# Kernel optimization log

Measured on AMD Instinct MI355X. Metric: run time of the kernel, lower is better.

## Reference

```python
import jax, jax.numpy as jnp
import numpy as np

IN_DIMS = 512
TOKEN_DIM = 512
NUM_HEADS = 1
D = TOKEN_DIM * NUM_HEADS
SCALE = TOKEN_DIM ** (-0.5)
EPS = 1e-12  # torch F.normalize default


def _l2norm(v, axis):
    n = jnp.sqrt(jnp.sum(v * v, axis=axis, keepdims=True))
    return v / jnp.maximum(n, EPS)


def setup_inputs() -> dict:
    key = jax.random.key(0)
    ks = jax.random.split(key, 10)
    B, C, H, W = 64, IN_DIMS, 28, 28
    s_in = IN_DIMS ** -0.5
    s_d = D ** -0.5
    return {
        "x": jax.random.normal(ks[0], (B, C, H, W), jnp.float32),
        "Wq": jax.random.normal(ks[1], (IN_DIMS, D), jnp.float32) * s_in,
        "bq": jax.random.normal(ks[2], (D,), jnp.float32) * 0.01,
        "Wk": jax.random.normal(ks[3], (IN_DIMS, D), jnp.float32) * s_in,
        "bk": jax.random.normal(ks[4], (D,), jnp.float32) * 0.01,
        "w_g": jax.random.normal(ks[5], (D, 1), jnp.float32),
        "Wp": jax.random.normal(ks[6], (D, D), jnp.float32) * s_d,
        "bp": jax.random.normal(ks[7], (D,), jnp.float32) * 0.01,
        "Wf": jax.random.normal(ks[8], (D, TOKEN_DIM), jnp.float32) * s_d,
        "bf": jax.random.normal(ks[9], (TOKEN_DIM,), jnp.float32) * 0.01,
    }


def reference(x, Wq, bq, Wk, bk, w_g, Wp, bp, Wf, bf):
    B, C, H, W = x.shape
    t = x.reshape(B, C, H * W).transpose(0, 2, 1)          # [B, N, C]
    query = _l2norm(t @ Wq + bq, axis=-1)                  # [B, N, D]
    k = _l2norm(t @ Wk + bk, axis=-1)                      # [B, N, D]
    attn = _l2norm((query @ w_g) * SCALE, axis=1)          # [B, N, 1], normalized over tokens
    ctx = jnp.sum(attn * query, axis=1, keepdims=True)     # [B, 1, D] global context
    out = (ctx * k) @ Wp + bp + query                      # [B, N, D]
    out = out @ Wf + bf                                    # [B, N, TOKEN_DIM]
    return out.transpose(0, 2, 1).reshape(B, -1, H, W)
```

## Files before the change

### kernel.cpp

```cpp
#include <hip/hip_runtime.h>

#define EPSN 1e-12f
#define SCALE_F 0.044194173824159216f

typedef __bf16 bf16x8 __attribute__((ext_vector_type(8)));
typedef __bf16 bf16x4 __attribute__((ext_vector_type(4)));
typedef float  f32x4  __attribute__((ext_vector_type(4)));

__device__ __forceinline__ void gld16(const void* src, void* dst) {
  __builtin_amdgcn_global_load_lds(
      (const __attribute__((address_space(1))) unsigned int*)src,
      (__attribute__((address_space(3))) unsigned int*)dst, 16, 0, 0);
}

__global__ __launch_bounds__(256) void k_prep_t(const float* __restrict__ Wq,
                                                const float* __restrict__ Wk,
                                                __bf16* __restrict__ WqT,
                                                __bf16* __restrict__ WkT) {
  __shared__ float Tq[32][33], Tk[32][33];
  const int c0 = blockIdx.x * 32, d0 = blockIdx.y * 32;
  const int dx = threadIdx.x, cy = threadIdx.y;
  #pragma unroll
  for (int p = 0; p < 4; ++p) {
    int c = cy + p * 8;
    Tq[c][dx] = Wq[(size_t)(c0 + c) * 512 + d0 + dx];
    Tk[c][dx] = Wk[(size_t)(c0 + c) * 512 + d0 + dx];
  }
  __syncthreads();
  #pragma unroll
  for (int p = 0; p < 4; ++p) {
    int d = cy + p * 8;
    WqT[(size_t)(d0 + d) * 512 + c0 + dx] = (__bf16)Tq[dx][d];
    WkT[(size_t)(d0 + d) * 512 + c0 + dx] = (__bf16)Tk[dx][d];
  }
}

__global__ __launch_bounds__(512) void k_prep_w(const float* __restrict__ Wp,
                                                const float* __restrict__ Wf,
                                                const float* __restrict__ bp,
                                                const float* __restrict__ bfv,
                                                __bf16* __restrict__ WcT,
                                                float* __restrict__ bpf) {
  int kk = blockIdx.x;
  int d  = threadIdx.x;
  float a0 = 0.f, a1 = 0.f, a2 = 0.f, a3 = 0.f;
  for (int c = 0; c < 512; c += 4) {
    a0 = fmaf(Wp[kk * 512 + c],     Wf[(size_t)c * 512 + d],         a0);
    a1 = fmaf(Wp[kk * 512 + c + 1], Wf[(size_t)(c + 1) * 512 + d],   a1);
    a2 = fmaf(Wp[kk * 512 + c + 2], Wf[(size_t)(c + 2) * 512 + d],   a2);
    a3 = fmaf(Wp[kk * 512 + c + 3], Wf[(size_t)(c + 3) * 512 + d],   a3);
  }
  WcT[(size_t)d * 1024 + kk]       = (__bf16)((a0 + a1) + (a2 + a3));
  WcT[(size_t)d * 1024 + 512 + kk] = (__bf16)Wf[(size_t)kk * 512 + d];
  if (kk == 0) {
    float b0 = 0.f, b1 = 0.f;
    for (int c = 0; c < 512; c += 2) {
      b0 = fmaf(bp[c],     Wf[(size_t)c * 512 + d],       b0);
      b1 = fmaf(bp[c + 1], Wf[(size_t)(c + 1) * 512 + d], b1);
    }
    bpf[d] = b0 + b1 + bfv[d];
  }
}

__global__ __launch_bounds__(512, 4) void k_qk(const float* __restrict__ x,
                                               const __bf16* __restrict__ WqT,
                                               const __bf16* __restrict__ WkT,
                                               const float* __restrict__ bq,
                                               const float* __restrict__ bk,
                                               const float* __restrict__ wg,
                                               __bf16* __restrict__ Qn,
                                               __bf16* __restrict__ Kn,
                                               float* __restrict__ pctx,
                                               float* __restrict__ pgsq) {
  __shared__ __align__(1024) unsigned char stg[36864];
  __shared__ float red[8][64], redG[8][64], invv[64], gs[64];
  const int t = threadIdx.x, lane = t & 63, w = t >> 6;
  const int li = lane & 15, lq = lane >> 4;
  const int n0 = blockIdx.x * 64, b = blockIdx.y, isK = blockIdx.z;
  const __bf16* Wt  = isK ? WkT : WqT;
  const float* bias = isK ? bk : bq;
  __bf16* dst       = isK ? Kn : Qn;

  const int stok = t & 63, scp = (t >> 6) * 4;
  const bool nv = (n0 + stok < 784);
  const float* xp = x + ((size_t)b * 512 + scp) * 784 + n0 + stok;
  const __bf16* wsrc = Wt + (size_t)((w * 4) * 16 + (lane >> 2)) * 512 + (lane & 3) * 8;

  f32x4 acc[4][4] = {};

  for (int ks = 0; ks < 16; ++ks) {
    const int k0 = ks * 32;
    #pragma unroll
    for (int i = 0; i < 4; ++i) {
      int r = w * 4 + i;
      gld16(wsrc + (size_t)i * 16 * 512 + k0, (void*)(stg + 4096 + r * 1024));
    }
    {
      float v0 = nv ? xp[(size_t)(k0 + 0) * 784] : 0.f;
      float v1 = nv ? xp[(size_t)(k0 + 1) * 784] : 0.f;
      float v2 = nv ? xp[(size_t)(k0 + 2) * 784] : 0.f;
      float v3 = nv ? xp[(size_t)(k0 + 3) * 784] : 0.f;
      bf16x4 v; v[0] = (__bf16)v0; v[1] = (__bf16)v1; v[2] = (__bf16)v2; v[3] = (__bf16)v3;
      *(bf16x4*)(stg + stok * 64 + scp * 2) = v;
    }
    __syncthreads();
    bf16x8 af[4];
    #pragma unroll
    for (int rb = 0; rb < 4; ++rb)
      af[rb] = *(const bf16x8*)(stg + (rb * 16 + li) * 64 + lq * 16);
    #pragma unroll
    for (int cb = 0; cb < 4; ++cb) {
      bf16x8 bf = *(const bf16x8*)(stg + 4096 + (w * 64 + cb * 16 + li) * 64 + lq * 16);
      #pragma unroll
      for (int rb = 0; rb < 4; ++rb)
        acc[rb][cb] = __builtin_amdgcn_mfma_f32_16x16x32_bf16(af[rb], bf, acc[rb][cb], 0, 0, 0);
    }
    __syncthreads();
  }

  float bv[4], wv[4];
  #pragma unroll
  for (int cb = 0; cb < 4; ++cb) {
    int col = w * 64 + cb * 16 + li;
    bv[cb] = bias[col];
    wv[cb] = isK ? 0.f : wg[col];
  }
  #pragma unroll
  for (int rb = 0; rb < 4; ++rb)
    #pragma unroll
    for (int cb = 0; cb < 4; ++cb)
      #pragma unroll
      for (int j = 0; j < 4; ++j)
        acc[rb][cb][j] += bv[cb];
  #pragma unroll
  for (int rb = 0; rb < 4; ++rb)
    #pragma unroll
    for (int j = 0; j < 4; ++j) {
      float ss = 0.f, sg = 0.f;
      #pragma unroll
      for (int cb = 0; cb < 4; ++cb) {
        float v = acc[rb][cb][j];
        ss = fmaf(v, v, ss); sg = fmaf(v, wv[cb], sg);
      }
      ss += __shfl_xor(ss, 1); ss += __shfl_xor(ss, 2); ss += __shfl_xor(ss, 4); ss += __shfl_xor(ss, 8);
      sg += __shfl_xor(sg, 1); sg += __shfl_xor(sg, 2); sg += __shfl_xor(sg, 4); sg += __shfl_xor(sg, 8);
      if (li == 0) {
        int row = rb * 16 + lq * 4 + j;
        red[w][row] = ss; redG[w][row] = sg;
      }
    }
  __syncthreads();
  if (t < 64) {
    float ss = 0.f, sg = 0.f;
    #pragma unroll
    for (int wv2 = 0; wv2 < 8; ++wv2) { ss += red[wv2][t]; sg += redG[wv2][t]; }
    float iv = 1.f / fmaxf(sqrtf(ss), EPSN);
    invv[t] = iv;
    if (!isK) {
      float gv = (n0 + t < 784) ? sg * iv : 0.f;
      gs[t] = gv;
      float pg = gv * gv;
      pg += __shfl_xor(pg, 1);  pg += __shfl_xor(pg, 2);  pg += __shfl_xor(pg, 4);
      pg += __shfl_xor(pg, 8);  pg += __shfl_xor(pg, 16); pg += __shfl_xor(pg, 32);
      if (t == 0) pgsq[b * 13 + blockIdx.x] = pg;
    }
  }
  __syncthreads();
  float pc[4] = {0.f, 0.f, 0.f, 0.f};
  #pragma unroll
  for (int rb = 0; rb < 4; ++rb)
    #pragma unroll
    for (int j = 0; j < 4; ++j) {
      int row = rb * 16 + lq * 4 + j;
      if (n0 + row < 784) {
        float iv = invv[row];
        float gr = isK ? 0.f : gs[row];
        size_t base = ((size_t)b * 784 + n0 + row) * 512 + w * 64 + li;
        #pragma unroll
        for (int cb = 0; cb < 4; ++cb) {
          float qv = acc[rb][cb][j] * iv;
          dst[base + cb * 16] = (__bf16)qv;
          pc[cb] = fmaf(gr, qv, pc[cb]);
        }
      }
    }
  if (!isK) {
    #pragma unroll
    for (int cb = 0; cb < 4; ++cb) {
      pc[cb] += __shfl_xor(pc[cb], 16);
      pc[cb] += __shfl_xor(pc[cb], 32);
    }
    if (lq == 0) {
      #pragma unroll
      for (int cb = 0; cb < 4; ++cb)
        pctx[((size_t)b * 13 + blockIdx.x) * 512 + w * 64 + cb * 16 + li] = pc[cb];
    }
  }
}

__global__ __launch_bounds__(512) void k_ctx2(const float* __restrict__ pctx,
                                              const float* __restrict__ pgsq,
                                              float* __restrict__ ctx) {
  const int b = blockIdx.x, t = threadIdx.x;
  float tot = 0.f;
  #pragma unroll
  for (int i = 0; i < 13; ++i) tot += pgsq[b * 13 + i];
  float alpha = SCALE_F / fmaxf(sqrtf(tot) * SCALE_F, EPSN);
  float s = 0.f;
  #pragma unroll
  for (int i = 0; i < 13; ++i) s += pctx[((size_t)b * 13 + i) * 512 + t];
  ctx[(size_t)b * 512 + t] = alpha * s;
}

__global__ __launch_bounds__(512) void k_kc(__bf16* __restrict__ Kn,
                                            const float* __restrict__ ctx) {
  const int b = blockIdx.y;
  const int chunk = blockIdx.x * 512 + threadIdx.x;
  const int row = chunk >> 6;
  const int c8 = (chunk & 63) * 8;
  __bf16* p = Kn + ((size_t)b * 784 + row) * 512 + c8;
  const float* cp = ctx + b * 512 + c8;
  bf16x8 v = *(const bf16x8*)p;
  #pragma unroll
  for (int j = 0; j < 8; ++j) v[j] = (__bf16)((float)v[j] * cp[j]);
  *(bf16x8*)p = v;
}

__global__ __launch_bounds__(512, 4) void k_out(const __bf16* __restrict__ Qn,
                                                const __bf16* __restrict__ Kc,
                                                const __bf16* __restrict__ WcT,
                                                const float* __restrict__ bpf,
                                                float* __restrict__ out) {
  __shared__ __align__(1024) unsigned char stg[36864];
  const int t = threadIdx.x, lane = t & 63, w = t >> 6;
  const int li = lane & 15, lq = lane >> 4;
  const int n0 = blockIdx.x * 64, b = blockIdx.y;
  size_t grow = (size_t)b * 784 + n0 + (lane >> 2);
  f32x4 acc[4][4] = {};

  for (int ks = 0; ks < 32; ++ks) {
    const int k0 = ks * 32;
    const __bf16* Arow = (ks < 16) ? Kc : Qn;
    const int kA = (ks < 16) ? k0 : k0 - 512;
    #pragma unroll
    for (int i = 0; i < 5; ++i) {
      int r = w + i * 8;
      if (r < 36) {
        void* dstl = (void*)(stg + r * 1024);
        if (r < 4) {
          size_t gr = grow + r * 16;
          if (gr > 50175) gr = 50175;
          gld16(Arow + gr * 512 + kA + (lane & 3) * 8, dstl);
        } else {
          int dr = (r - 4) * 16 + (lane >> 2);
          gld16(WcT + (size_t)dr * 1024 + k0 + (lane & 3) * 8, dstl);
        }
      }
    }
    __syncthreads();
    bf16x8 af[4];
    #pragma unroll
    for (int rb = 0; rb < 4; ++rb)
      af[rb] = *(const bf16x8*)(stg + (rb * 16 + li) * 64 + lq * 16);
    #pragma unroll
    for (int cb = 0; cb < 4; ++cb) {
      bf16x8 bf = *(const bf16x8*)(stg + 4096 + (w * 64 + cb * 16 + li) * 64 + lq * 16);
      #pragma unroll
      for (int rb = 0; rb < 4; ++rb)
        acc[rb][cb] = __builtin_amdgcn_mfma_f32_16x16x32_bf16(af[rb], bf, acc[rb][cb], 0, 0, 0);
    }
    __syncthreads();
  }

  float bv[4];
  #pragma unroll
  for (int cb = 0; cb < 4; ++cb) bv[cb] = bpf[w * 64 + cb * 16 + li];
  #pragma unroll
  for (int rb = 0; rb < 4; ++rb) {
    int nrow = n0 + rb * 16 + lq * 4;
    if (nrow < 784) {
      #pragma unroll
      for (int cb = 0; cb < 4; ++cb) {
        f32x4 v;
        #pragma unroll
        for (int j = 0; j < 4; ++j) v[j] = acc[rb][cb][j] + bv[cb];
        *(f32x4*)&out[((size_t)b * 512 + w * 64 + cb * 16 + li) * 784 + nrow] = v;
      }
    }
  }
}

extern "C" void kernel_launch(void* const* d_in, const int* in_sizes, int n_in,
                              void* d_out, int out_size, void* d_ws, size_t ws_size,
                              hipStream_t stream) {
  const float* x   = (const float*)d_in[0];
  const float* Wq  = (const float*)d_in[1];
  const float* bq  = (const float*)d_in[2];
  const float* Wk  = (const float*)d_in[3];
  const float* bk  = (const float*)d_in[4];
  const float* wg  = (const float*)d_in[5];
  const float* Wp  = (const float*)d_in[6];
  const float* bp  = (const float*)d_in[7];
  const float* Wf  = (const float*)d_in[8];
  const float* bfv = (const float*)d_in[9];
  float* out = (float*)d_out;
  char* ws = (char*)d_ws;

  const size_t SZQN = (size_t)64 * 784 * 512 * 2;
  __bf16* Qn   = (__bf16*)(ws);
  __bf16* Kn   = (__bf16*)(ws + SZQN);
  __bf16* WqT  = (__bf16*)(ws + 2 * SZQN);
  __bf16* WkT  = (__bf16*)(ws + 2 * SZQN + 524288);
  __bf16* WcT  = (__bf16*)(ws + 2 * SZQN + 2 * 524288);
  float*  bpf  = (float*) (ws + 2 * SZQN + 2 * 524288 + 1048576);
  float*  pctx = (float*) (ws + 2 * SZQN + 2 * 524288 + 1048576 + 2048);
  float*  pgsq = (float*) (ws + 2 * SZQN + 2 * 524288 + 1048576 + 2048 + 1703936);
  float*  ctx  = (float*) (ws + 2 * SZQN + 2 * 524288 + 1048576 + 2048 + 1703936 + 4096);

  k_prep_t<<<dim3(16, 16),    dim3(32, 8), 0, stream>>>(Wq, Wk, WqT, WkT);
  k_prep_w<<<dim3(512),       dim3(512),   0, stream>>>(Wp, Wf, bp, bfv, WcT, bpf);
  k_qk    <<<dim3(13, 64, 2), dim3(512),   0, stream>>>(x, WqT, WkT, bq, bk, wg, Qn, Kn, pctx, pgsq);
  k_ctx2  <<<dim3(64),        dim3(512),   0, stream>>>(pctx, pgsq, ctx);
  k_kc    <<<dim3(98, 64),    dim3(512),   0, stream>>>(Kn, ctx);
  k_out   <<<dim3(13, 64),    dim3(512),   0, stream>>>(Qn, Kn, WcT, bpf, out);
}
```

Baseline: 347.2 us.

## Retile QK and output GEMMs to 128x128 tiles with deferred normalization

```diff
diff --git a/kernel.cpp b/kernel.cpp
--- a/kernel.cpp
+++ b/kernel.cpp
@@ -2,6 +2,7 @@
 
 #define EPSN 1e-12f
 #define SCALE_F 0.044194173824159216f
+#define MTOT 50176
 
 typedef __bf16 bf16x8 __attribute__((ext_vector_type(8)));
 typedef __bf16 bf16x4 __attribute__((ext_vector_type(4)));
@@ -41,76 +42,82 @@
                                                 const float* __restrict__ bfv,
                                                 __bf16* __restrict__ WcT,
                                                 float* __restrict__ bpf) {
-  int kk = blockIdx.x;
-  int d  = threadIdx.x;
-  float a0 = 0.f, a1 = 0.f, a2 = 0.f, a3 = 0.f;
-  for (int c = 0; c < 512; c += 4) {
-    a0 = fmaf(Wp[kk * 512 + c],     Wf[(size_t)c * 512 + d],         a0);
-    a1 = fmaf(Wp[kk * 512 + c + 1], Wf[(size_t)(c + 1) * 512 + d],   a1);
-    a2 = fmaf(Wp[kk * 512 + c + 2], Wf[(size_t)(c + 2) * 512 + d],   a2);
-    a3 = fmaf(Wp[kk * 512 + c + 3], Wf[(size_t)(c + 3) * 512 + d],   a3);
-  }
-  WcT[(size_t)d * 1024 + kk]       = (__bf16)((a0 + a1) + (a2 + a3));
-  WcT[(size_t)d * 1024 + 512 + kk] = (__bf16)Wf[(size_t)kk * 512 + d];
-  if (kk == 0) {
-    float b0 = 0.f, b1 = 0.f;
-    for (int c = 0; c < 512; c += 2) {
-      b0 = fmaf(bp[c],     Wf[(size_t)c * 512 + d],       b0);
-      b1 = fmaf(bp[c + 1], Wf[(size_t)(c + 1) * 512 + d], b1);
-    }
-    bpf[d] = b0 + b1 + bfv[d];
-  }
-}
-
-__global__ __launch_bounds__(512, 4) void k_qk(const float* __restrict__ x,
-                                               const __bf16* __restrict__ WqT,
-                                               const __bf16* __restrict__ WkT,
-                                               const float* __restrict__ bq,
-                                               const float* __restrict__ bk,
-                                               const float* __restrict__ wg,
-                                               __bf16* __restrict__ Qn,
-                                               __bf16* __restrict__ Kn,
-                                               float* __restrict__ pctx,
-                                               float* __restrict__ pgsq) {
-  __shared__ __align__(1024) unsigned char stg[36864];
-  __shared__ float red[8][64], redG[8][64], invv[64], gs[64];
-  const int t = threadIdx.x, lane = t & 63, w = t >> 6;
-  const int li = lane & 15, lq = lane >> 4;
-  const int n0 = blockIdx.x * 64, b = blockIdx.y, isK = blockIdx.z;
-  const __bf16* Wt  = isK ? WkT : WqT;
-  const float* bias = isK ? bk : bq;
-  __bf16* dst       = isK ? Kn : Qn;
-
-  const int stok = t & 63, scp = (t >> 6) * 4;
-  const bool nv = (n0 + stok < 784);
-  const float* xp = x + ((size_t)b * 512 + scp) * 784 + n0 + stok;
-  const __bf16* wsrc = Wt + (size_t)((w * 4) * 16 + (lane >> 2)) * 512 + (lane & 3) * 8;
+  const int kk0 = blockIdx.x * 8;
+  const int d = threadIdx.x;
+  float acc[8] = {};
+  float bacc = 0.f;
+  const bool dobp = (blockIdx.x == 0);
+  for (int c = 0; c < 512; ++c) {
+    float wf = Wf[(size_t)c * 512 + d];
+    #pragma unroll
+    for (int i = 0; i < 8; ++i) acc[i] = fmaf(Wp[(size_t)(kk0 + i) * 512 + c], wf, acc[i]);
+    if (dobp) bacc = fmaf(bp[c], wf, bacc);
+  }
+  #pragma unroll
+  for (int i = 0; i < 8; ++i) {
+    WcT[(size_t)d * 1024 + kk0 + i]       = (__bf16)acc[i];
+    WcT[(size_t)d * 1024 + 512 + kk0 + i] = (__bf16)Wf[(size_t)(kk0 + i) * 512 + d];
+  }
+  if (dobp) bpf[d] = bacc + bfv[d];
+}
+
+__global__ __launch_bounds__(256, 3) void k_gemm(const float* __restrict__ x,
+                                                 const __bf16* __restrict__ WqT,
+                                                 const __bf16* __restrict__ WkT,
+                                                 const float* __restrict__ bq,
+                                                 const float* __restrict__ bk,
+                                                 const float* __restrict__ wg,
+                                                 __bf16* __restrict__ qraw,
+                                                 __bf16* __restrict__ kraw,
+                                                 float* __restrict__ psqQ,
+                                                 float* __restrict__ psqK,
+                                                 float* __restrict__ gdo) {
+  __shared__ __align__(1024) unsigned char As[8192], Bs[8192];
+  const int t = threadIdx.x, l = t & 63, w = t >> 6;
+  const int li = l & 15, lq = l >> 4;
+  const int p = blockIdx.x;
+  const int xq = p & 7, q2 = p >> 3;
+  const int m8 = q2 & 7;
+  const int g = (q2 >> 3) * 8 + xq;
+  const int b = g / 7, mt = g % 7;
+  const int qk = m8 >> 2, nt = m8 & 3;
+  const int m0 = mt * 128;
+  const __bf16* Wt = qk ? WkT : WqT;
+
+  const int r0 = 2 * w, r1 = r0 + 1;
+  int row0 = m0 + r0 * 16 + li; if (row0 > 783) row0 = 783;
+  int row1 = m0 + r1 * 16 + li; if (row1 > 783) row1 = 783;
+  const float* xp0 = x + ((size_t)b * 512 + lq * 8) * 784 + row0;
+  const float* xp1 = x + ((size_t)b * 512 + lq * 8) * 784 + row1;
+  const __bf16* wp0 = Wt + (size_t)(nt * 128 + r0 * 16 + li) * 512 + lq * 8;
+  const __bf16* wp1 = Wt + (size_t)(nt * 128 + r1 * 16 + li) * 512 + lq * 8;
 
   f32x4 acc[4][4] = {};
 
   for (int ks = 0; ks < 16; ++ks) {
     const int k0 = ks * 32;
-    #pragma unroll
-    for (int i = 0; i < 4; ++i) {
-      int r = w * 4 + i;
-      gld16(wsrc + (size_t)i * 16 * 512 + k0, (void*)(stg + 4096 + r * 1024));
-    }
+    gld16(wp0 + k0, Bs + r0 * 1024);
+    gld16(wp1 + k0, Bs + r1 * 1024);
     {
-      float v0 = nv ? xp[(size_t)(k0 + 0) * 784] : 0.f;
-      float v1 = nv ? xp[(size_t)(k0 + 1) * 784] : 0.f;
-      float v2 = nv ? xp[(size_t)(k0 + 2) * 784] : 0.f;
-      float v3 = nv ? xp[(size_t)(k0 + 3) * 784] : 0.f;
-      bf16x4 v; v[0] = (__bf16)v0; v[1] = (__bf16)v1; v[2] = (__bf16)v2; v[3] = (__bf16)v3;
-      *(bf16x4*)(stg + stok * 64 + scp * 2) = v;
+      float v0[8], v1[8];
+      #pragma unroll
+      for (int j = 0; j < 8; ++j) v0[j] = xp0[(size_t)(k0 + j) * 784];
+      #pragma unroll
+      for (int j = 0; j < 8; ++j) v1[j] = xp1[(size_t)(k0 + j) * 784];
+      bf16x8 a0, a1;
+      #pragma unroll
+      for (int j = 0; j < 8; ++j) { a0[j] = (__bf16)v0[j]; a1[j] = (__bf16)v1[j]; }
+      *(bf16x8*)(As + r0 * 1024 + l * 16) = a0;
+      *(bf16x8*)(As + r1 * 1024 + l * 16) = a1;
     }
     __syncthreads();
     bf16x8 af[4];
     #pragma unroll
     for (int rb = 0; rb < 4; ++rb)
-      af[rb] = *(const bf16x8*)(stg + (rb * 16 + li) * 64 + lq * 16);
+      af[rb] = *(const bf16x8*)(As + ((w & 1) * 4 + rb) * 1024 + l * 16);
     #pragma unroll
     for (int cb = 0; cb < 4; ++cb) {
-      bf16x8 bf = *(const bf16x8*)(stg + 4096 + (w * 64 + cb * 16 + li) * 64 + lq * 16);
+      bf16x8 bf = *(const bf16x8*)(Bs + ((w >> 1) * 4 + cb) * 1024 + l * 16);
       #pragma unroll
       for (int rb = 0; rb < 4; ++rb)
         acc[rb][cb] = __builtin_amdgcn_mfma_f32_16x16x32_bf16(af[rb], bf, acc[rb][cb], 0, 0, 0);
@@ -118,153 +125,169 @@
     __syncthreads();
   }
 
+  const float* bias = qk ? bk : bq;
+  __bf16* dst = qk ? kraw : qraw;
+  float* psq = qk ? psqK : psqQ;
+  const int colb = nt * 128 + (w >> 1) * 64;
+  const int cg = nt * 2 + (w >> 1);
   float bv[4], wv[4];
   #pragma unroll
   for (int cb = 0; cb < 4; ++cb) {
-    int col = w * 64 + cb * 16 + li;
+    int col = colb + cb * 16 + li;
     bv[cb] = bias[col];
-    wv[cb] = isK ? 0.f : wg[col];
+    wv[cb] = qk ? 0.f : wg[col];
   }
   #pragma unroll
   for (int rb = 0; rb < 4; ++rb)
     #pragma unroll
-    for (int cb = 0; cb < 4; ++cb)
-      #pragma unroll
-      for (int j = 0; j < 4; ++j)
-        acc[rb][cb][j] += bv[cb];
-  #pragma unroll
-  for (int rb = 0; rb < 4; ++rb)
-    #pragma unroll
     for (int j = 0; j < 4; ++j) {
+      int rowg = m0 + (w & 1) * 64 + rb * 16 + lq * 4 + j;
+      bool ok = rowg < 784;
+      size_t token = (size_t)b * 784 + rowg;
       float ss = 0.f, sg = 0.f;
       #pragma unroll
       for (int cb = 0; cb < 4; ++cb) {
-        float v = acc[rb][cb][j];
-        ss = fmaf(v, v, ss); sg = fmaf(v, wv[cb], sg);
+        float v = acc[rb][cb][j] + bv[cb];
+        ss = fmaf(v, v, ss);
+        sg = fmaf(v, wv[cb], sg);
+        if (ok) dst[token * 512 + colb + cb * 16 + li] = (__bf16)v;
       }
       ss += __shfl_xor(ss, 1); ss += __shfl_xor(ss, 2); ss += __shfl_xor(ss, 4); ss += __shfl_xor(ss, 8);
       sg += __shfl_xor(sg, 1); sg += __shfl_xor(sg, 2); sg += __shfl_xor(sg, 4); sg += __shfl_xor(sg, 8);
-      if (li == 0) {
-        int row = rb * 16 + lq * 4 + j;
-        red[w][row] = ss; redG[w][row] = sg;
+      if (ok && li == 0) {
+        psq[(size_t)cg * MTOT + token] = ss;
+        if (!qk) gdo[(size_t)cg * MTOT + token] = sg;
       }
     }
+}
+
+__global__ __launch_bounds__(256) void k_normc(const float* __restrict__ psqQ,
+                                               const float* __restrict__ psqK,
+                                               const float* __restrict__ gdo,
+                                               float* __restrict__ invqA,
+                                               float* __restrict__ invkA,
+                                               float* __restrict__ coefA,
+                                               float* __restrict__ gA) {
+  const int tkn = blockIdx.x * 256 + threadIdx.x;
+  if (tkn >= MTOT) return;
+  float sq = 0.f, sk = 0.f, gd = 0.f;
+  #pragma unroll
+  for (int cg = 0; cg < 8; ++cg) {
+    sq += psqQ[(size_t)cg * MTOT + tkn];
+    sk += psqK[(size_t)cg * MTOT + tkn];
+    gd += gdo[(size_t)cg * MTOT + tkn];
+  }
+  float invq = 1.f / fmaxf(sqrtf(sq), EPSN);
+  float invk = 1.f / fmaxf(sqrtf(sk), EPSN);
+  float gv = gd * invq;
+  invqA[tkn] = invq;
+  invkA[tkn] = invk;
+  coefA[tkn] = gv * invq;
+  gA[tkn]    = gv;
+}
+
+__global__ __launch_bounds__(512) void k_pctx(const __bf16* __restrict__ qraw,
+                                              const float* __restrict__ coefA,
+                                              const float* __restrict__ gA,
+                                              float* __restrict__ ctx) {
+  __shared__ float wred[8];
+  const int b = blockIdx.x, t = threadIdx.x;
+  const size_t base = (size_t)b * 784;
+  float gsq = 0.f;
+  { float gv = gA[base + t]; gsq = gv * gv; }
+  if (t + 512 < 784) { float gv = gA[base + t + 512]; gsq = fmaf(gv, gv, gsq); }
+  gsq += __shfl_xor(gsq, 1);  gsq += __shfl_xor(gsq, 2);  gsq += __shfl_xor(gsq, 4);
+  gsq += __shfl_xor(gsq, 8);  gsq += __shfl_xor(gsq, 16); gsq += __shfl_xor(gsq, 32);
+  if ((t & 63) == 0) wred[t >> 6] = gsq;
   __syncthreads();
-  if (t < 64) {
-    float ss = 0.f, sg = 0.f;
-    #pragma unroll
-    for (int wv2 = 0; wv2 < 8; ++wv2) { ss += red[wv2][t]; sg += redG[wv2][t]; }
-    float iv = 1.f / fmaxf(sqrtf(ss), EPSN);
-    invv[t] = iv;
-    if (!isK) {
-      float gv = (n0 + t < 784) ? sg * iv : 0.f;
-      gs[t] = gv;
-      float pg = gv * gv;
-      pg += __shfl_xor(pg, 1);  pg += __shfl_xor(pg, 2);  pg += __shfl_xor(pg, 4);
-      pg += __shfl_xor(pg, 8);  pg += __shfl_xor(pg, 16); pg += __shfl_xor(pg, 32);
-      if (t == 0) pgsq[b * 13 + blockIdx.x] = pg;
-    }
-  }
-  __syncthreads();
-  float pc[4] = {0.f, 0.f, 0.f, 0.f};
-  #pragma unroll
-  for (int rb = 0; rb < 4; ++rb)
-    #pragma unroll
-    for (int j = 0; j < 4; ++j) {
-      int row = rb * 16 + lq * 4 + j;
-      if (n0 + row < 784) {
-        float iv = invv[row];
-        float gr = isK ? 0.f : gs[row];
-        size_t base = ((size_t)b * 784 + n0 + row) * 512 + w * 64 + li;
-        #pragma unroll
-        for (int cb = 0; cb < 4; ++cb) {
-          float qv = acc[rb][cb][j] * iv;
-          dst[base + cb * 16] = (__bf16)qv;
-          pc[cb] = fmaf(gr, qv, pc[cb]);
-        }
-      }
-    }
-  if (!isK) {
-    #pragma unroll
-    for (int cb = 0; cb < 4; ++cb) {
-      pc[cb] += __shfl_xor(pc[cb], 16);
-      pc[cb] += __shfl_xor(pc[cb], 32);
-    }
-    if (lq == 0) {
-      #pragma unroll
-      for (int cb = 0; cb < 4; ++cb)
-        pctx[((size_t)b * 13 + blockIdx.x) * 512 + w * 64 + cb * 16 + li] = pc[cb];
-    }
-  }
-}
-
-__global__ __launch_bounds__(512) void k_ctx2(const float* __restrict__ pctx,
-                                              const float* __restrict__ pgsq,
-                                              float* __restrict__ ctx) {
-  const int b = blockIdx.x, t = threadIdx.x;
   float tot = 0.f;
   #pragma unroll
-  for (int i = 0; i < 13; ++i) tot += pgsq[b * 13 + i];
-  float alpha = SCALE_F / fmaxf(sqrtf(tot) * SCALE_F, EPSN);
-  float s = 0.f;
-  #pragma unroll
-  for (int i = 0; i < 13; ++i) s += pctx[((size_t)b * 13 + i) * 512 + t];
-  ctx[(size_t)b * 512 + t] = alpha * s;
-}
-
-__global__ __launch_bounds__(512) void k_kc(__bf16* __restrict__ Kn,
-                                            const float* __restrict__ ctx) {
-  const int b = blockIdx.y;
-  const int chunk = blockIdx.x * 512 + threadIdx.x;
-  const int row = chunk >> 6;
-  const int c8 = (chunk & 63) * 8;
-  __bf16* p = Kn + ((size_t)b * 784 + row) * 512 + c8;
-  const float* cp = ctx + b * 512 + c8;
-  bf16x8 v = *(const bf16x8*)p;
-  #pragma unroll
-  for (int j = 0; j < 8; ++j) v[j] = (__bf16)((float)v[j] * cp[j]);
-  *(bf16x8*)p = v;
-}
-
-__global__ __launch_bounds__(512, 4) void k_out(const __bf16* __restrict__ Qn,
-                                                const __bf16* __restrict__ Kc,
+  for (int i = 0; i < 8; ++i) tot += wred[i];
+  const float alpha = SCALE_F / fmaxf(sqrtf(tot) * SCALE_F, EPSN);
+  float a0 = 0.f, a1 = 0.f, a2 = 0.f, a3 = 0.f;
+  for (int n = 0; n < 784; n += 4) {
+    a0 = fmaf(coefA[base + n],     (float)qraw[(base + n) * 512 + t],     a0);
+    a1 = fmaf(coefA[base + n + 1], (float)qraw[(base + n + 1) * 512 + t], a1);
+    a2 = fmaf(coefA[base + n + 2], (float)qraw[(base + n + 2) * 512 + t], a2);
+    a3 = fmaf(coefA[base + n + 3], (float)qraw[(base + n + 3) * 512 + t], a3);
+  }
+  ctx[(size_t)b * 512 + t] = alpha * ((a0 + a1) + (a2 + a3));
+}
+
+__global__ __launch_bounds__(256, 3) void k_out(const __bf16* __restrict__ qraw,
+                                                const __bf16* __restrict__ kraw,
+                                                const float* __restrict__ invqA,
+                                                const float* __restrict__ invkA,
+                                                const float* __restrict__ ctx,
                                                 const __bf16* __restrict__ WcT,
                                                 const float* __restrict__ bpf,
                                                 float* __restrict__ out) {
-  __shared__ __align__(1024) unsigned char stg[36864];
-  const int t = threadIdx.x, lane = t & 63, w = t >> 6;
-  const int li = lane & 15, lq = lane >> 4;
-  const int n0 = blockIdx.x * 64, b = blockIdx.y;
-  size_t grow = (size_t)b * 784 + n0 + (lane >> 2);
+  __shared__ __align__(1024) unsigned char As[8192], Bs[8192];
+  __shared__ float ctx_l[512];
+  const int t = threadIdx.x, l = t & 63, w = t >> 6;
+  const int li = l & 15, lq = l >> 4;
+  const int p = blockIdx.x;
+  const int xq = p & 7, q2 = p >> 3;
+  const int nt = q2 & 3;
+  const int g = (q2 >> 2) * 8 + xq;
+  const int b = g / 7, mt = g % 7;
+  const int m0 = mt * 128;
+
+  ctx_l[t]       = ctx[(size_t)b * 512 + t];
+  ctx_l[t + 256] = ctx[(size_t)b * 512 + t + 256];
+
+  const int rA0 = w, rA1 = w + 4;
+  int row0 = m0 + rA0 * 16 + li; if (row0 > 783) row0 = 783;
+  int row1 = m0 + rA1 * 16 + li; if (row1 > 783) row1 = 783;
+  const size_t tk0 = (size_t)b * 784 + row0, tk1 = (size_t)b * 784 + row1;
+  const float iq0 = invqA[tk0], ik0 = invkA[tk0];
+  const float iq1 = invqA[tk1], ik1 = invkA[tk1];
+  const __bf16* wpB0 = WcT + (size_t)(nt * 128 + (2 * w) * 16 + li) * 1024 + lq * 8;
+  const __bf16* wpB1 = WcT + (size_t)(nt * 128 + (2 * w + 1) * 16 + li) * 1024 + lq * 8;
+
   f32x4 acc[4][4] = {};
+  __syncthreads();
 
   for (int ks = 0; ks < 32; ++ks) {
     const int k0 = ks * 32;
-    const __bf16* Arow = (ks < 16) ? Kc : Qn;
-    const int kA = (ks < 16) ? k0 : k0 - 512;
-    #pragma unroll
-    for (int i = 0; i < 5; ++i) {
-      int r = w + i * 8;
-      if (r < 36) {
-        void* dstl = (void*)(stg + r * 1024);
-        if (r < 4) {
-          size_t gr = grow + r * 16;
-          if (gr > 50175) gr = 50175;
-          gld16(Arow + gr * 512 + kA + (lane & 3) * 8, dstl);
-        } else {
-          int dr = (r - 4) * 16 + (lane >> 2);
-          gld16(WcT + (size_t)dr * 1024 + k0 + (lane & 3) * 8, dstl);
+    gld16(wpB0 + k0, Bs + (2 * w) * 1024);
+    gld16(wpB1 + k0, Bs + (2 * w + 1) * 1024);
+    {
+      const bool dk = ks < 16;
+      const __bf16* ap = dk ? kraw : qraw;
+      const int kk = (k0 & 511) + lq * 8;
+      bf16x8 v0 = *(const bf16x8*)(ap + tk0 * 512 + kk);
+      bf16x8 v1 = *(const bf16x8*)(ap + tk1 * 512 + kk);
+      const float s0 = dk ? ik0 : iq0, s1 = dk ? ik1 : iq1;
+      bf16x8 o0, o1;
+      if (dk) {
+        f32x4 c0 = *(const f32x4*)&ctx_l[kk];
+        f32x4 c1 = *(const f32x4*)&ctx_l[kk + 4];
+        #pragma unroll
+        for (int j = 0; j < 4; ++j) {
+          o0[j]     = (__bf16)((float)v0[j]     * s0 * c0[j]);
+          o0[4 + j] = (__bf16)((float)v0[4 + j] * s0 * c1[j]);
+          o1[j]     = (__bf16)((float)v1[j]     * s1 * c0[j]);
+          o1[4 + j] = (__bf16)((float)v1[4 + j] * s1 * c1[j]);
+        }
+      } else {
+        #pragma unroll
+        for (int j = 0; j < 8; ++j) {
+          o0[j] = (__bf16)((float)v0[j] * s0);
+          o1[j] = (__bf16)((float)v1[j] * s1);
         }
       }
+      *(bf16x8*)(As + rA0 * 1024 + l * 16) = o0;
+      *(bf16x8*)(As + rA1 * 1024 + l * 16) = o1;
     }
     __syncthreads();
     bf16x8 af[4];
     #pragma unroll
     for (int rb = 0; rb < 4; ++rb)
-      af[rb] = *(const bf16x8*)(stg + (rb * 16 + li) * 64 + lq * 16);
+      af[rb] = *(const bf16x8*)(As + ((w & 1) * 4 + rb) * 1024 + l * 16);
     #pragma unroll
     for (int cb = 0; cb < 4; ++cb) {
-      bf16x8 bf = *(const bf16x8*)(stg + 4096 + (w * 64 + cb * 16 + li) * 64 + lq * 16);
+      bf16x8 bf = *(const bf16x8*)(Bs + ((w >> 1) * 4 + cb) * 1024 + l * 16);
       #pragma unroll
       for (int rb = 0; rb < 4; ++rb)
         acc[rb][cb] = __builtin_amdgcn_mfma_f32_16x16x32_bf16(af[rb], bf, acc[rb][cb], 0, 0, 0);
@@ -272,19 +295,20 @@
     __syncthreads();
   }
 
+  const int colb = nt * 128 + (w >> 1) * 64;
   float bv[4];
   #pragma unroll
-  for (int cb = 0; cb < 4; ++cb) bv[cb] = bpf[w * 64 + cb * 16 + li];
+  for (int cb = 0; cb < 4; ++cb) bv[cb] = bpf[colb + cb * 16 + li];
   #pragma unroll
   for (int rb = 0; rb < 4; ++rb) {
-    int nrow = n0 + rb * 16 + lq * 4;
+    int nrow = m0 + (w & 1) * 64 + rb * 16 + lq * 4;
     if (nrow < 784) {
       #pragma unroll
       for (int cb = 0; cb < 4; ++cb) {
         f32x4 v;
         #pragma unroll
         for (int j = 0; j < 4; ++j) v[j] = acc[rb][cb][j] + bv[cb];
-        *(f32x4*)&out[((size_t)b * 512 + w * 64 + cb * 16 + li) * 784 + nrow] = v;
+        *(f32x4*)&out[((size_t)b * 512 + colb + cb * 16 + li) * 784 + nrow] = v;
       }
     }
   }
@@ -306,21 +330,28 @@
   float* out = (float*)d_out;
   char* ws = (char*)d_ws;
 
-  const size_t SZQN = (size_t)64 * 784 * 512 * 2;
-  __bf16* Qn   = (__bf16*)(ws);
-  __bf16* Kn   = (__bf16*)(ws + SZQN);
-  __bf16* WqT  = (__bf16*)(ws + 2 * SZQN);
-  __bf16* WkT  = (__bf16*)(ws + 2 * SZQN + 524288);
-  __bf16* WcT  = (__bf16*)(ws + 2 * SZQN + 2 * 524288);
-  float*  bpf  = (float*) (ws + 2 * SZQN + 2 * 524288 + 1048576);
-  float*  pctx = (float*) (ws + 2 * SZQN + 2 * 524288 + 1048576 + 2048);
-  float*  pgsq = (float*) (ws + 2 * SZQN + 2 * 524288 + 1048576 + 2048 + 1703936);
-  float*  ctx  = (float*) (ws + 2 * SZQN + 2 * 524288 + 1048576 + 2048 + 1703936 + 4096);
-
-  k_prep_t<<<dim3(16, 16),    dim3(32, 8), 0, stream>>>(Wq, Wk, WqT, WkT);
-  k_prep_w<<<dim3(512),       dim3(512),   0, stream>>>(Wp, Wf, bp, bfv, WcT, bpf);
-  k_qk    <<<dim3(13, 64, 2), dim3(512),   0, stream>>>(x, WqT, WkT, bq, bk, wg, Qn, Kn, pctx, pgsq);
-  k_ctx2  <<<dim3(64),        dim3(512),   0, stream>>>(pctx, pgsq, ctx);
-  k_kc    <<<dim3(98, 64),    dim3(512),   0, stream>>>(Kn, ctx);
-  k_out   <<<dim3(13, 64),    dim3(512),   0, stream>>>(Qn, Kn, WcT, bpf, out);
-}
+  const size_t SZRAW = (size_t)MTOT * 512 * 2;
+  size_t off = 0;
+  __bf16* qraw = (__bf16*)(ws + off); off += SZRAW;
+  __bf16* kraw = (__bf16*)(ws + off); off += SZRAW;
+  __bf16* WqT  = (__bf16*)(ws + off); off += 524288;
+  __bf16* WkT  = (__bf16*)(ws + off); off += 524288;
+  __bf16* WcT  = (__bf16*)(ws + off); off += 1048576;
+  float*  bpf  = (float*) (ws + off); off += 2048;
+  float*  psqQ = (float*) (ws + off); off += (size_t)8 * MTOT * 4;
+  float*  psqK = (float*) (ws + off); off += (size_t)8 * MTOT * 4;
+  float*  gdo  = (float*) (ws + off); off += (size_t)8 * MTOT * 4;
+  float*  invqA = (float*)(ws + off); off += (size_t)MTOT * 4;
+  float*  invkA = (float*)(ws + off); off += (size_t)MTOT * 4;
+  float*  coefA = (float*)(ws + off); off += (size_t)MTOT * 4;
+  float*  gA    = (float*)(ws + off); off += (size_t)MTOT * 4;
+  float*  ctx   = (float*)(ws + off); off += 131072;
+
+  k_prep_t<<<dim3(16, 16), dim3(32, 8), 0, stream>>>(Wq, Wk, WqT, WkT);
+  k_prep_w<<<dim3(64),     dim3(512),   0, stream>>>(Wp, Wf, bp, bfv, WcT, bpf);
+  k_gemm  <<<dim3(3584),   dim3(256),   0, stream>>>(x, WqT, WkT, bq, bk, wg,
+                                                     qraw, kraw, psqQ, psqK, gdo);
+  k_normc <<<dim3(196),    dim3(256),   0, stream>>>(psqQ, psqK, gdo, invqA, invkA, coefA, gA);
+  k_pctx  <<<dim3(64),     dim3(512),   0, stream>>>(qraw, coefA, gA, ctx);
+  k_out   <<<dim3(1792),   dim3(256),   0, stream>>>(qraw, kraw, invqA, invkA, ctx, WcT, bpf, out);
+}
```

New measurement: 411.3 us. 18.5% more time.
